# Performance work log

Measured on AMD Instinct MI355X. Metric: run time of the kernel, lower is better.

## Reference

```python
import jax, jax.numpy as jnp
import numpy as np

N = 200_000   # nodes
E = 6_400_000 # edges (avg degree 32)


def setup_inputs() -> dict:
    key = jax.random.key(0)
    k = jax.random.split(key, 6)
    x = jax.random.normal(k[0], (N, 2), dtype=jnp.float32)
    edge_index = jax.random.randint(k[1], (2, E), 0, N, dtype=jnp.int32)
    # GCNConv(2, 8) and GCNConv(8, 4) parameters (Glorot-ish init, zero bias as in PyG)
    W1 = jax.random.normal(k[2], (2, 8), dtype=jnp.float32) * (1.0 / np.sqrt(2.0))
    b1 = jnp.zeros((8,), dtype=jnp.float32)
    W2 = jax.random.normal(k[3], (8, 4), dtype=jnp.float32) * (1.0 / np.sqrt(8.0))
    b2 = jnp.zeros((4,), dtype=jnp.float32)
    return {"x": x, "edge_index": edge_index, "W1": W1, "b1": b1, "W2": W2, "b2": b2}


def _gcn_conv(x, src, dst, norm, W, b, n):
    # PyG GCNConv: linear transform, normalized gather/scatter-add, bias after aggregation
    h = x @ W                                   # [N, F_out]
    msg = h[src] * norm[:, None]                # gather + edge-wise scale, [E', F_out]
    agg = jax.ops.segment_sum(msg, dst, num_segments=n)  # scatter-add at targets
    return agg + b


def reference(x, edge_index, W1, b1, W2, b2):
    n = x.shape[0]
    # add self-loops (PyG default add_self_loops=True)
    loops = jnp.arange(n, dtype=edge_index.dtype)
    src = jnp.concatenate([edge_index[0], loops])
    dst = jnp.concatenate([edge_index[1], loops])
    # symmetric degree normalization: deg computed at targets with unit edge weights
    deg = jax.ops.segment_sum(jnp.ones_like(src, dtype=x.dtype), dst, num_segments=n)
    deg_inv_sqrt = jnp.where(deg > 0, jax.lax.rsqrt(jnp.maximum(deg, 1.0)), 0.0)
    norm = deg_inv_sqrt[src] * deg_inv_sqrt[dst]  # [E']

    h = jax.nn.relu(_gcn_conv(x, src, dst, norm, W1, b1, n))
    out = _gcn_conv(h, src, dst, norm, W2, b2, n)
    return out
```

## Files before the change

kernel.cpp:

```cpp
#include <hip/hip_runtime.h>


#define EPB   8192
#define PART  2048
#define LPBIT 11
#define SRCB  18
#define BC    4
#define RSTR  2049
#define STCAP 17408


__global__ __launch_bounds__(512) void countA_kernel(
    const int* __restrict__ dst, int* __restrict__ cntmat, int E, int P) {
    __shared__ int cnt[128];
    int tid = threadIdx.x;
    if (tid < 128) cnt[tid] = 0;
    __syncthreads();
    int nv4 = E >> 2;
    int b4 = (blockIdx.x * EPB) >> 2;
    int e4 = min(b4 + (EPB >> 2), nv4);
    const int4* d4 = (const int4*)dst;
    #pragma unroll
    for (int k = 0; k < (EPB >> 2); k += 512) {
        int i = b4 + k + tid;
        if (i < e4) {
            int4 d = d4[i];
            atomicAdd(&cnt[d.x >> LPBIT], 1);
            atomicAdd(&cnt[d.y >> LPBIT], 1);
            atomicAdd(&cnt[d.z >> LPBIT], 1);
            atomicAdd(&cnt[d.w >> LPBIT], 1);
        }
    }
    if (blockIdx.x == gridDim.x - 1) {
        int e = (nv4 << 2) + tid;
        if (e < E) atomicAdd(&cnt[dst[e] >> LPBIT], 1);
    }
    __syncthreads();
    int* row = cntmat + (size_t)blockIdx.x * P;
    if (tid < P) row[tid] = cnt[tid];
}

__global__ __launch_bounds__(256) void colscanA_kernel(
    int* __restrict__ cntmat, int* __restrict__ colTotal, int B, int P) {
    __shared__ int sdata[256];
    int p = blockIdx.x, tid = threadIdx.x;
    int v[4];
    int s = 0;
    #pragma unroll
    for (int k = 0; k < 4; k++) {
        int b = tid * 4 + k;
        v[k] = (b < B) ? cntmat[(size_t)b * P + p] : 0;
        s += v[k];
    }
    int x = s;
    sdata[tid] = x;
    __syncthreads();
    for (int off = 1; off < 256; off <<= 1) {
        int t = (tid >= off) ? sdata[tid - off] : 0;
        __syncthreads();
        x += t;
        sdata[tid] = x;
        __syncthreads();
    }
    int run = x - s;
    #pragma unroll
    for (int k = 0; k < 4; k++) {
        int b = tid * 4 + k;
        if (b < B) cntmat[(size_t)b * P + p] = run;
        run += v[k];
    }
    if (tid == 255) colTotal[p] = x;
}

__global__ __launch_bounds__(256) void totalscanA_kernel(
    const int* __restrict__ colTotal, int* __restrict__ colStart,
    int P, int E) {
    __shared__ int sdata[256];
    int tid = threadIdx.x;
    int v[4];
    int s = 0;
    #pragma unroll
    for (int k = 0; k < 4; k++) {
        int i = tid * 4 + k;
        v[k] = (i < P) ? colTotal[i] : 0;
        s += v[k];
    }
    int x = s;
    sdata[tid] = x;
    __syncthreads();
    for (int off = 1; off < 256; off <<= 1) {
        int t = (tid >= off) ? sdata[tid - off] : 0;
        __syncthreads();
        x += t;
        sdata[tid] = x;
        __syncthreads();
    }
    int run = x - s;
    #pragma unroll
    for (int k = 0; k < 4; k++) {
        int i = tid * 4 + k;
        if (i < P) colStart[i] = run;
        run += v[k];
    }
    if (tid == 0) colStart[P] = E;
}

__global__ __launch_bounds__(512) void scatterA_kernel(
    const int* __restrict__ src, const int* __restrict__ dst,
    const int* __restrict__ cntmat, const int* __restrict__ colStart,
    unsigned* __restrict__ packed, int E, int P) {
    __shared__ int cur[128];
    int tid = threadIdx.x;
    if (tid < P) cur[tid] = colStart[tid] + cntmat[(size_t)blockIdx.x * P + tid];
    __syncthreads();
    int nv4 = E >> 2;
    int b4 = (blockIdx.x * EPB) >> 2;
    int e4 = min(b4 + (EPB >> 2), nv4);
    const int4* d4 = (const int4*)dst;
    const int4* s4 = (const int4*)src;
    #pragma unroll
    for (int k = 0; k < (EPB >> 2); k += 512) {
        int i = b4 + k + tid;
        if (i < e4) {
            int4 d = d4[i];
            int4 sv = s4[i];
            int p0 = atomicAdd(&cur[d.x >> LPBIT], 1);
            packed[p0] = ((unsigned)(d.x & (PART - 1)) << SRCB) | (unsigned)sv.x;
            int p1 = atomicAdd(&cur[d.y >> LPBIT], 1);
            packed[p1] = ((unsigned)(d.y & (PART - 1)) << SRCB) | (unsigned)sv.y;
            int p2 = atomicAdd(&cur[d.z >> LPBIT], 1);
            packed[p2] = ((unsigned)(d.z & (PART - 1)) << SRCB) | (unsigned)sv.z;
            int p3 = atomicAdd(&cur[d.w >> LPBIT], 1);
            packed[p3] = ((unsigned)(d.w & (PART - 1)) << SRCB) | (unsigned)sv.w;
        }
    }
    if (blockIdx.x == gridDim.x - 1) {
        int e = (nv4 << 2) + tid;
        if (e < E) {
            int d = dst[e];
            int pos = atomicAdd(&cur[d >> LPBIT], 1);
            packed[pos] = ((unsigned)(d & (PART - 1)) << SRCB) | (unsigned)src[e];
        }
    }
}


__global__ __launch_bounds__(512) void localC_kernel(
    const unsigned* __restrict__ packed, const int* __restrict__ colStart,
    int* __restrict__ runStart, int* __restrict__ srcsorted) {
    __shared__ int hist[PART];
    __shared__ int sdata[512];
    __shared__ unsigned stage[STCAP];
    int tid = threadIdx.x;
    int dp = blockIdx.x >> 2, b = blockIdx.x & (BC - 1);
    int s0 = colStart[dp], len = colStart[dp + 1] - s0;
    int lo = s0 + (int)(((long long)len * b) / BC);
    int hi = s0 + (int)(((long long)len * (b + 1)) / BC);
    for (int k = tid; k < PART; k += 512) hist[k] = 0;
    __syncthreads();
    for (int i = lo + tid; i < hi; i += 512)
        atomicAdd(&hist[packed[i] >> SRCB], 1);
    __syncthreads();
    int off = tid * 4;
    int v0 = hist[off], v1 = hist[off + 1], v2 = hist[off + 2], v3 = hist[off + 3];
    int s = v0 + v1 + v2 + v3;
    int x = s;
    sdata[tid] = x;
    __syncthreads();
    for (int o = 1; o < 512; o <<= 1) {
        int t = (tid >= o) ? sdata[tid - o] : 0;
        __syncthreads();
        x += t;
        sdata[tid] = x;
        __syncthreads();
    }
    int run = x - s;
    int* rs = runStart + (size_t)(dp * BC + b) * RSTR;
    int c0 = lo + run, c1 = c0 + v0, c2 = c1 + v1, c3 = c2 + v2;
    rs[off] = c0; rs[off + 1] = c1; rs[off + 2] = c2; rs[off + 3] = c3;
    __syncthreads();
    hist[off] = c0; hist[off + 1] = c1; hist[off + 2] = c2; hist[off + 3] = c3;
    if (tid == 0) rs[PART] = hi;
    __syncthreads();
    int total = hi - lo;
    bool ovf = total > STCAP;
    for (int i = lo + tid; i < hi; i += 512) {
        unsigned w = packed[i];
        int pos = atomicAdd(&hist[w >> SRCB], 1);
        unsigned sv = w & ((1u << SRCB) - 1);
        if (!ovf) stage[pos - lo] = sv;
        else srcsorted[pos] = sv;
    }
    __syncthreads();
    if (!ovf)
        for (int j = tid; j < total; j += 512) srcsorted[lo + j] = (int)stage[j];
}


__global__ __launch_bounds__(512) void dinvg_kernel(
    const int* __restrict__ runStart, const float* __restrict__ x,
    float* __restrict__ dinv, float* __restrict__ g, int n) {
    int i = blockIdx.x * 512 + threadIdx.x;
    if (i >= n) return;
    int dp = i >> LPBIT, ld = i & (PART - 1);
    int deg = 0;
    #pragma unroll
    for (int b = 0; b < BC; b++) {
        const int* rs = runStart + (size_t)(dp * BC + b) * RSTR + ld;
        deg += rs[1] - rs[0];
    }
    float d = rsqrtf((float)deg + 1.0f);
    dinv[i] = d;
    float2 xv = ((const float2*)x)[i];
    ((float2*)g)[i] = make_float2(xv.x * d, xv.y * d);
}

__global__ __launch_bounds__(512) void agg1_kernel(
    const int* __restrict__ runStart, const int* __restrict__ srcsorted,
    const float* __restrict__ g, const float* __restrict__ dinv,
    const float* __restrict__ W1, const float* __restrict__ b1,
    const float* __restrict__ W2, float* __restrict__ hs2, int n) {
    int i = blockIdx.x * 512 + threadIdx.x;
    if (i >= n) return;
    int dp = i >> LPBIT, ld = i & (PART - 1);
    const float2* gp = (const float2*)g;
    float s0 = 0.0f, s1 = 0.0f;
    #pragma unroll
    for (int b = 0; b < BC; b++) {
        const int* rs = runStart + (size_t)(dp * BC + b) * RSTR + ld;
        int p0 = rs[0], p1 = rs[1];
        int p = p0;
        for (; p + 4 <= p1; p += 4) {
            int a = srcsorted[p], bb = srcsorted[p + 1];
            int c = srcsorted[p + 2], e = srcsorted[p + 3];
            float2 w0 = gp[a], w1 = gp[bb], w2 = gp[c], w3 = gp[e];
            s0 += w0.x + w1.x + w2.x + w3.x;
            s1 += w0.y + w1.y + w2.y + w3.y;
        }
        for (; p < p1; p++) {
            float2 w = gp[srcsorted[p]];
            s0 += w.x;
            s1 += w.y;
        }
    }
    float d = dinv[i];
    float2 gi = gp[i];
    s0 = (s0 + gi.x) * d;
    s1 = (s1 + gi.y) * d;
    float h[8];
    #pragma unroll
    for (int f = 0; f < 8; f++)
        h[f] = fmaxf(s0 * W1[f] + s1 * W1[8 + f] + b1[f], 0.0f);
    float oc[4];
    #pragma unroll
    for (int k = 0; k < 4; k++) {
        float a = 0.0f;
        #pragma unroll
        for (int f = 0; f < 8; f++) a += h[f] * W2[4 * f + k];
        oc[k] = a * d;
    }
    float4 o;
    o.x = oc[0]; o.y = oc[1]; o.z = oc[2]; o.w = oc[3];
    *(float4*)(hs2 + 4 * (size_t)i) = o;
}

__global__ __launch_bounds__(512) void agg2_kernel(
    const int* __restrict__ runStart, const int* __restrict__ srcsorted,
    const float* __restrict__ hs2, const float* __restrict__ dinv,
    const float* __restrict__ b2, float* __restrict__ out, int n) {
    int i = blockIdx.x * 512 + threadIdx.x;
    if (i >= n) return;
    int dp = i >> LPBIT, ld = i & (PART - 1);
    const float4* hp = (const float4*)hs2;
    float s0 = 0.0f, s1 = 0.0f, s2 = 0.0f, s3 = 0.0f;
    #pragma unroll
    for (int b = 0; b < BC; b++) {
        const int* rs = runStart + (size_t)(dp * BC + b) * RSTR + ld;
        int p0 = rs[0], p1 = rs[1];
        int p = p0;
        for (; p + 4 <= p1; p += 4) {
            int a = srcsorted[p], bb = srcsorted[p + 1];
            int c = srcsorted[p + 2], e = srcsorted[p + 3];
            float4 w0 = hp[a], w1 = hp[bb], w2 = hp[c], w3 = hp[e];
            s0 += w0.x + w1.x + w2.x + w3.x;
            s1 += w0.y + w1.y + w2.y + w3.y;
            s2 += w0.z + w1.z + w2.z + w3.z;
            s3 += w0.w + w1.w + w2.w + w3.w;
        }
        for (; p < p1; p++) {
            float4 w = hp[srcsorted[p]];
            s0 += w.x; s1 += w.y; s2 += w.z; s3 += w.w;
        }
    }
    float d = dinv[i];
    float4 hi2 = hp[i];
    float4 o;
    o.x = d * (s0 + hi2.x) + b2[0];
    o.y = d * (s1 + hi2.y) + b2[1];
    o.z = d * (s2 + hi2.z) + b2[2];
    o.w = d * (s3 + hi2.w) + b2[3];
    *(float4*)(out + 4 * (size_t)i) = o;
}

extern "C" void kernel_launch(void* const* d_in, const int* in_sizes, int n_in,
                              void* d_out, int out_size, void* d_ws, size_t ws_size,
                              hipStream_t stream) {
    const float* x   = (const float*)d_in[0];
    const int*   ei  = (const int*)d_in[1];
    const float* W1  = (const float*)d_in[2];
    const float* b1  = (const float*)d_in[3];
    const float* W2  = (const float*)d_in[4];
    const float* b2  = (const float*)d_in[5];
    float* out = (float*)d_out;

    const int n = in_sizes[0] / 2;
    const int E = in_sizes[1] / 2;
    const int* src = ei;
    const int* dst = ei + E;

    const int P  = (n + PART - 1) >> LPBIT;
    const int B1 = (E + EPB - 1) / EPB;

    int* ws = (int*)d_ws;
    int* colTotal = ws;
    int* colStart = ws + 1024;
    int* cntmatA  = ws + 2048;
    size_t cmsz = (((size_t)B1 * P) + 3) & ~(size_t)3;
    int* runStart = cntmatA + cmsz;
    size_t rssz = (((size_t)P * BC * RSTR) + 3) & ~(size_t)3;
    unsigned* packed = (unsigned*)(runStart + rssz);
    int* srcsorted = (int*)(packed + E);
    size_t nd = (size_t)P << LPBIT;
    float* dinv = (float*)packed;
    float* g    = dinv + nd;
    float* hs2  = g + 2 * nd;

    const int gN = (n + 511) / 512;

    countA_kernel    <<<B1, 512, 0, stream>>>(dst, cntmatA, E, P);
    colscanA_kernel  <<<P, 256, 0, stream>>>(cntmatA, colTotal, B1, P);
    totalscanA_kernel<<<1, 256, 0, stream>>>(colTotal, colStart, P, E);
    scatterA_kernel  <<<B1, 512, 0, stream>>>(src, dst, cntmatA, colStart, packed, E, P);
    localC_kernel    <<<P * BC, 512, 0, stream>>>(packed, colStart, runStart, srcsorted);
    dinvg_kernel     <<<gN, 512, 0, stream>>>(runStart, x, dinv, g, n);
    agg1_kernel      <<<gN, 512, 0, stream>>>(runStart, srcsorted, g, dinv, W1, b1, W2, hs2, n);
    agg2_kernel      <<<gN, 512, 0, stream>>>(runStart, srcsorted, hs2, dinv, b2, out, n);
}
```

Baseline: 247.6 us.

## Split each node's aggregation across four lanes, one per source bucket

The two aggregation kernels now assign four threads per destination node, each walking one of the BC=4 source-bucket runs. Partial sums are combined with xor shuffles, and each lane writes one output feature. The aim is four times more parallelism and more independent gathers in flight, which should hide latency better on the random-gather-bound loops. The cost is redundant per-node work (the dense W1/W2 math is repeated per lane), scalar instead of float4 stores, and more divergence when run lengths differ.

```diff
diff --git a/kernel.cpp b/kernel.cpp
--- a/kernel.cpp
+++ b/kernel.cpp
@@ -220,86 +220,79 @@
     const float* __restrict__ g, const float* __restrict__ dinv,
     const float* __restrict__ W1, const float* __restrict__ b1,
     const float* __restrict__ W2, float* __restrict__ hs2, int n) {
-    int i = blockIdx.x * 512 + threadIdx.x;
+    int t = blockIdx.x * 512 + threadIdx.x;
+    int i = t >> 2;
     if (i >= n) return;
+    int b = t & 3;
     int dp = i >> LPBIT, ld = i & (PART - 1);
+    const int* rs = runStart + (size_t)(dp * BC + b) * RSTR + ld;
+    int p0 = rs[0], p1 = rs[1];
     const float2* gp = (const float2*)g;
     float s0 = 0.0f, s1 = 0.0f;
-    #pragma unroll
-    for (int b = 0; b < BC; b++) {
-        const int* rs = runStart + (size_t)(dp * BC + b) * RSTR + ld;
-        int p0 = rs[0], p1 = rs[1];
-        int p = p0;
-        for (; p + 4 <= p1; p += 4) {
-            int a = srcsorted[p], bb = srcsorted[p + 1];
-            int c = srcsorted[p + 2], e = srcsorted[p + 3];
-            float2 w0 = gp[a], w1 = gp[bb], w2 = gp[c], w3 = gp[e];
-            s0 += w0.x + w1.x + w2.x + w3.x;
-            s1 += w0.y + w1.y + w2.y + w3.y;
-        }
-        for (; p < p1; p++) {
-            float2 w = gp[srcsorted[p]];
-            s0 += w.x;
-            s1 += w.y;
-        }
-    }
+    int p = p0;
+    for (; p + 4 <= p1; p += 4) {
+        int a = srcsorted[p], bb = srcsorted[p + 1];
+        int c = srcsorted[p + 2], e = srcsorted[p + 3];
+        float2 w0 = gp[a], w1 = gp[bb], w2 = gp[c], w3 = gp[e];
+        s0 += w0.x + w1.x + w2.x + w3.x;
+        s1 += w0.y + w1.y + w2.y + w3.y;
+    }
+    for (; p < p1; p++) {
+        float2 w = gp[srcsorted[p]];
+        s0 += w.x;
+        s1 += w.y;
+    }
+    s0 += __shfl_xor(s0, 1); s0 += __shfl_xor(s0, 2);
+    s1 += __shfl_xor(s1, 1); s1 += __shfl_xor(s1, 2);
     float d = dinv[i];
     float2 gi = gp[i];
     s0 = (s0 + gi.x) * d;
     s1 = (s1 + gi.y) * d;
-    float h[8];
-    #pragma unroll
-    for (int f = 0; f < 8; f++)
-        h[f] = fmaxf(s0 * W1[f] + s1 * W1[8 + f] + b1[f], 0.0f);
-    float oc[4];
-    #pragma unroll
-    for (int k = 0; k < 4; k++) {
-        float a = 0.0f;
-        #pragma unroll
-        for (int f = 0; f < 8; f++) a += h[f] * W2[4 * f + k];
-        oc[k] = a * d;
-    }
-    float4 o;
-    o.x = oc[0]; o.y = oc[1]; o.z = oc[2]; o.w = oc[3];
-    *(float4*)(hs2 + 4 * (size_t)i) = o;
+    float acc = 0.0f;
+    #pragma unroll
+    for (int f = 0; f < 8; f++) {
+        float h = fmaxf(s0 * W1[f] + s1 * W1[8 + f] + b1[f], 0.0f);
+        acc += h * W2[4 * f + b];
+    }
+    hs2[4 * (size_t)i + b] = acc * d;
 }
 
 __global__ __launch_bounds__(512) void agg2_kernel(
     const int* __restrict__ runStart, const int* __restrict__ srcsorted,
     const float* __restrict__ hs2, const float* __restrict__ dinv,
     const float* __restrict__ b2, float* __restrict__ out, int n) {
-    int i = blockIdx.x * 512 + threadIdx.x;
+    int t = blockIdx.x * 512 + threadIdx.x;
+    int i = t >> 2;
     if (i >= n) return;
+    int b = t & 3;
     int dp = i >> LPBIT, ld = i & (PART - 1);
+    const int* rs = runStart + (size_t)(dp * BC + b) * RSTR + ld;
+    int p0 = rs[0], p1 = rs[1];
     const float4* hp = (const float4*)hs2;
     float s0 = 0.0f, s1 = 0.0f, s2 = 0.0f, s3 = 0.0f;
-    #pragma unroll
-    for (int b = 0; b < BC; b++) {
-        const int* rs = runStart + (size_t)(dp * BC + b) * RSTR + ld;
-        int p0 = rs[0], p1 = rs[1];
-        int p = p0;
-        for (; p + 4 <= p1; p += 4) {
-            int a = srcsorted[p], bb = srcsorted[p + 1];
-            int c = srcsorted[p + 2], e = srcsorted[p + 3];
-            float4 w0 = hp[a], w1 = hp[bb], w2 = hp[c], w3 = hp[e];
-            s0 += w0.x + w1.x + w2.x + w3.x;
-            s1 += w0.y + w1.y + w2.y + w3.y;
-            s2 += w0.z + w1.z + w2.z + w3.z;
-            s3 += w0.w + w1.w + w2.w + w3.w;
-        }
-        for (; p < p1; p++) {
-            float4 w = hp[srcsorted[p]];
-            s0 += w.x; s1 += w.y; s2 += w.z; s3 += w.w;
-        }
-    }
+    int p = p0;
+    for (; p + 4 <= p1; p += 4) {
+        int a = srcsorted[p], bb = srcsorted[p + 1];
+        int c = srcsorted[p + 2], e = srcsorted[p + 3];
+        float4 w0 = hp[a], w1 = hp[bb], w2 = hp[c], w3 = hp[e];
+        s0 += w0.x + w1.x + w2.x + w3.x;
+        s1 += w0.y + w1.y + w2.y + w3.y;
+        s2 += w0.z + w1.z + w2.z + w3.z;
+        s3 += w0.w + w1.w + w2.w + w3.w;
+    }
+    for (; p < p1; p++) {
+        float4 w = hp[srcsorted[p]];
+        s0 += w.x; s1 += w.y; s2 += w.z; s3 += w.w;
+    }
+    s0 += __shfl_xor(s0, 1); s0 += __shfl_xor(s0, 2);
+    s1 += __shfl_xor(s1, 1); s1 += __shfl_xor(s1, 2);
+    s2 += __shfl_xor(s2, 1); s2 += __shfl_xor(s2, 2);
+    s3 += __shfl_xor(s3, 1); s3 += __shfl_xor(s3, 2);
     float d = dinv[i];
     float4 hi2 = hp[i];
-    float4 o;
-    o.x = d * (s0 + hi2.x) + b2[0];
-    o.y = d * (s1 + hi2.y) + b2[1];
-    o.z = d * (s2 + hi2.z) + b2[2];
-    o.w = d * (s3 + hi2.w) + b2[3];
-    *(float4*)(out + 4 * (size_t)i) = o;
+    float sb = (b == 0) ? s0 : (b == 1) ? s1 : (b == 2) ? s2 : s3;
+    float hb = (b == 0) ? hi2.x : (b == 1) ? hi2.y : (b == 2) ? hi2.z : hi2.w;
+    out[4 * (size_t)i + b] = d * (sb + hb) + b2[b];
 }
 
 extern "C" void kernel_launch(void* const* d_in, const int* in_sizes, int n_in,
@@ -335,7 +328,8 @@
     float* g    = dinv + nd;
     float* hs2  = g + 2 * nd;
 
-    const int gN = (n + 511) / 512;
+    const int gN  = (n + 511) / 512;
+    const int gN4 = (4 * n + 511) / 512;
 
     countA_kernel    <<<B1, 512, 0, stream>>>(dst, cntmatA, E, P);
     colscanA_kernel  <<<P, 256, 0, stream>>>(cntmatA, colTotal, B1, P);
@@ -343,6 +337,6 @@
     scatterA_kernel  <<<B1, 512, 0, stream>>>(src, dst, cntmatA, colStart, packed, E, P);
     localC_kernel    <<<P * BC, 512, 0, stream>>>(packed, colStart, runStart, srcsorted);
     dinvg_kernel     <<<gN, 512, 0, stream>>>(runStart, x, dinv, g, n);
-    agg1_kernel      <<<gN, 512, 0, stream>>>(runStart, srcsorted, g, dinv, W1, b1, W2, hs2, n);
-    agg2_kernel      <<<gN, 512, 0, stream>>>(runStart, srcsorted, hs2, dinv, b2, out, n);
-}
+    agg1_kernel      <<<gN4, 512, 0, stream>>>(runStart, srcsorted, g, dinv, W1, b1, W2, hs2, n);
+    agg2_kernel      <<<gN4, 512, 0, stream>>>(runStart, srcsorted, hs2, dinv, b2, out, n);
+}
```

Measured after the change: 248.5 us. No clear change (+0.4%).

## Switch aggregation from node-parallel CSR loops to edge-parallel segmented scans

Applied to the files above, without the earlier changes.

The sort output now keeps the packed destination-local id alongside the source id. Each aggregation is split into an edge-parallel kernel and a node kernel. The edge kernel finds each edge's partition by binary search over colStart, gathers the source features, reduces runs with equal destination using a wavefront shfl_up segmented scan, and emits one float atomicAdd per run. This removes the load imbalance and serial per-node loops of the node-parallel version, at the cost of extra accumulator zeroing, atomics, non-deterministic float summation order, and two more launches.

```diff
diff --git a/kernel.cpp b/kernel.cpp
--- a/kernel.cpp
+++ b/kernel.cpp
@@ -147,7 +147,7 @@
 
 __global__ __launch_bounds__(512) void localC_kernel(
     const unsigned* __restrict__ packed, const int* __restrict__ colStart,
-    int* __restrict__ runStart, int* __restrict__ srcsorted) {
+    int* __restrict__ runStart, int* __restrict__ sorted) {
     __shared__ int hist[PART];
     __shared__ int sdata[512];
     __shared__ unsigned stage[STCAP];
@@ -187,19 +187,19 @@
     for (int i = lo + tid; i < hi; i += 512) {
         unsigned w = packed[i];
         int pos = atomicAdd(&hist[w >> SRCB], 1);
-        unsigned sv = w & ((1u << SRCB) - 1);
-        if (!ovf) stage[pos - lo] = sv;
-        else srcsorted[pos] = sv;
+        if (!ovf) stage[pos - lo] = w;
+        else sorted[pos] = (int)w;
     }
     __syncthreads();
     if (!ovf)
-        for (int j = tid; j < total; j += 512) srcsorted[lo + j] = (int)stage[j];
+        for (int j = tid; j < total; j += 512) sorted[lo + j] = (int)stage[j];
 }
 
 
 __global__ __launch_bounds__(512) void dinvg_kernel(
     const int* __restrict__ runStart, const float* __restrict__ x,
-    float* __restrict__ dinv, float* __restrict__ g, int n) {
+    float* __restrict__ dinv, float* __restrict__ g,
+    float* __restrict__ acc1, float* __restrict__ acc2, int n) {
     int i = blockIdx.x * 512 + threadIdx.x;
     if (i >= n) return;
     int dp = i >> LPBIT, ld = i & (PART - 1);
@@ -213,93 +213,127 @@
     dinv[i] = d;
     float2 xv = ((const float2*)x)[i];
     ((float2*)g)[i] = make_float2(xv.x * d, xv.y * d);
-}
-
-__global__ __launch_bounds__(512) void agg1_kernel(
-    const int* __restrict__ runStart, const int* __restrict__ srcsorted,
-    const float* __restrict__ g, const float* __restrict__ dinv,
-    const float* __restrict__ W1, const float* __restrict__ b1,
-    const float* __restrict__ W2, float* __restrict__ hs2, int n) {
+    ((float2*)acc1)[i] = make_float2(0.0f, 0.0f);
+    ((float4*)acc2)[i] = make_float4(0.0f, 0.0f, 0.0f, 0.0f);
+}
+
+
+__global__ __launch_bounds__(512) void agg1e_kernel(
+    const int* __restrict__ sorted, const int* __restrict__ colStart,
+    const float* __restrict__ g, float* __restrict__ acc1, int E, int P) {
+    __shared__ int cs[132];
+    int tid = threadIdx.x;
+    for (int k = tid; k <= P; k += 512) cs[k] = colStart[k];
+    __syncthreads();
+    int e = blockIdx.x * 512 + tid;
+    int lane = tid & 63;
+    int sid = -1;
+    float s0 = 0.0f, s1 = 0.0f;
+    if (e < E) {
+        unsigned w = (unsigned)sorted[e];
+        int lo = 0, hi = P;
+        while (hi - lo > 1) { int mid = (lo + hi) >> 1; if (e >= cs[mid]) lo = mid; else hi = mid; }
+        sid = (lo << LPBIT) | (int)(w >> SRCB);
+        int src = (int)(w & ((1u << SRCB) - 1));
+        float2 gv = ((const float2*)g)[src];
+        s0 = gv.x; s1 = gv.y;
+    }
+    #pragma unroll
+    for (int off = 1; off < 64; off <<= 1) {
+        int ps = __shfl_up(sid, off);
+        float p0 = __shfl_up(s0, off);
+        float p1 = __shfl_up(s1, off);
+        if (lane >= off && ps == sid) { s0 += p0; s1 += p1; }
+    }
+    int ns = __shfl_down(sid, 1);
+    bool tail = (lane == 63) || (ns != sid);
+    if (tail && sid >= 0) {
+        atomicAdd(&acc1[2 * (size_t)sid],     s0);
+        atomicAdd(&acc1[2 * (size_t)sid + 1], s1);
+    }
+}
+
+__global__ __launch_bounds__(512) void agg2e_kernel(
+    const int* __restrict__ sorted, const int* __restrict__ colStart,
+    const float* __restrict__ hs2, float* __restrict__ acc2, int E, int P) {
+    __shared__ int cs[132];
+    int tid = threadIdx.x;
+    for (int k = tid; k <= P; k += 512) cs[k] = colStart[k];
+    __syncthreads();
+    int e = blockIdx.x * 512 + tid;
+    int lane = tid & 63;
+    int sid = -1;
+    float s0 = 0.0f, s1 = 0.0f, s2 = 0.0f, s3 = 0.0f;
+    if (e < E) {
+        unsigned w = (unsigned)sorted[e];
+        int lo = 0, hi = P;
+        while (hi - lo > 1) { int mid = (lo + hi) >> 1; if (e >= cs[mid]) lo = mid; else hi = mid; }
+        sid = (lo << LPBIT) | (int)(w >> SRCB);
+        int src = (int)(w & ((1u << SRCB) - 1));
+        float4 hv = ((const float4*)hs2)[src];
+        s0 = hv.x; s1 = hv.y; s2 = hv.z; s3 = hv.w;
+    }
+    #pragma unroll
+    for (int off = 1; off < 64; off <<= 1) {
+        int ps = __shfl_up(sid, off);
+        float p0 = __shfl_up(s0, off);
+        float p1 = __shfl_up(s1, off);
+        float p2 = __shfl_up(s2, off);
+        float p3 = __shfl_up(s3, off);
+        if (lane >= off && ps == sid) { s0 += p0; s1 += p1; s2 += p2; s3 += p3; }
+    }
+    int ns = __shfl_down(sid, 1);
+    bool tail = (lane == 63) || (ns != sid);
+    if (tail && sid >= 0) {
+        atomicAdd(&acc2[4 * (size_t)sid],     s0);
+        atomicAdd(&acc2[4 * (size_t)sid + 1], s1);
+        atomicAdd(&acc2[4 * (size_t)sid + 2], s2);
+        atomicAdd(&acc2[4 * (size_t)sid + 3], s3);
+    }
+}
+
+
+__global__ __launch_bounds__(512) void node1_kernel(
+    const float* __restrict__ acc1, const float* __restrict__ g,
+    const float* __restrict__ dinv, const float* __restrict__ W1,
+    const float* __restrict__ b1, const float* __restrict__ W2,
+    float* __restrict__ hs2, int n) {
     int i = blockIdx.x * 512 + threadIdx.x;
     if (i >= n) return;
-    int dp = i >> LPBIT, ld = i & (PART - 1);
-    const float2* gp = (const float2*)g;
-    float s0 = 0.0f, s1 = 0.0f;
-    #pragma unroll
-    for (int b = 0; b < BC; b++) {
-        const int* rs = runStart + (size_t)(dp * BC + b) * RSTR + ld;
-        int p0 = rs[0], p1 = rs[1];
-        int p = p0;
-        for (; p + 4 <= p1; p += 4) {
-            int a = srcsorted[p], bb = srcsorted[p + 1];
-            int c = srcsorted[p + 2], e = srcsorted[p + 3];
-            float2 w0 = gp[a], w1 = gp[bb], w2 = gp[c], w3 = gp[e];
-            s0 += w0.x + w1.x + w2.x + w3.x;
-            s1 += w0.y + w1.y + w2.y + w3.y;
-        }
-        for (; p < p1; p++) {
-            float2 w = gp[srcsorted[p]];
-            s0 += w.x;
-            s1 += w.y;
-        }
-    }
     float d = dinv[i];
-    float2 gi = gp[i];
-    s0 = (s0 + gi.x) * d;
-    s1 = (s1 + gi.y) * d;
-    float h[8];
-    #pragma unroll
-    for (int f = 0; f < 8; f++)
-        h[f] = fmaxf(s0 * W1[f] + s1 * W1[8 + f] + b1[f], 0.0f);
-    float oc[4];
-    #pragma unroll
-    for (int k = 0; k < 4; k++) {
-        float a = 0.0f;
-        #pragma unroll
-        for (int f = 0; f < 8; f++) a += h[f] * W2[4 * f + k];
-        oc[k] = a * d;
+    float2 a = ((const float2*)acc1)[i];
+    float2 gi = ((const float2*)g)[i];
+    float s0 = (a.x + gi.x) * d;
+    float s1 = (a.y + gi.y) * d;
+    float oc0 = 0.0f, oc1 = 0.0f, oc2 = 0.0f, oc3 = 0.0f;
+    #pragma unroll
+    for (int f = 0; f < 8; f++) {
+        float h = fmaxf(s0 * W1[f] + s1 * W1[8 + f] + b1[f], 0.0f);
+        oc0 += h * W2[4 * f];
+        oc1 += h * W2[4 * f + 1];
+        oc2 += h * W2[4 * f + 2];
+        oc3 += h * W2[4 * f + 3];
     }
     float4 o;
-    o.x = oc[0]; o.y = oc[1]; o.z = oc[2]; o.w = oc[3];
-    *(float4*)(hs2 + 4 * (size_t)i) = o;
-}
-
-__global__ __launch_bounds__(512) void agg2_kernel(
-    const int* __restrict__ runStart, const int* __restrict__ srcsorted,
-    const float* __restrict__ hs2, const float* __restrict__ dinv,
-    const float* __restrict__ b2, float* __restrict__ out, int n) {
+    o.x = oc0 * d; o.y = oc1 * d; o.z = oc2 * d; o.w = oc3 * d;
+    ((float4*)hs2)[i] = o;
+}
+
+__global__ __launch_bounds__(512) void node2_kernel(
+    const float* __restrict__ acc2, const float* __restrict__ hs2,
+    const float* __restrict__ dinv, const float* __restrict__ b2,
+    float* __restrict__ out, int n) {
     int i = blockIdx.x * 512 + threadIdx.x;
     if (i >= n) return;
-    int dp = i >> LPBIT, ld = i & (PART - 1);
-    const float4* hp = (const float4*)hs2;
-    float s0 = 0.0f, s1 = 0.0f, s2 = 0.0f, s3 = 0.0f;
-    #pragma unroll
-    for (int b = 0; b < BC; b++) {
-        const int* rs = runStart + (size_t)(dp * BC + b) * RSTR + ld;
-        int p0 = rs[0], p1 = rs[1];
-        int p = p0;
-        for (; p + 4 <= p1; p += 4) {
-            int a = srcsorted[p], bb = srcsorted[p + 1];
-            int c = srcsorted[p + 2], e = srcsorted[p + 3];
-            float4 w0 = hp[a], w1 = hp[bb], w2 = hp[c], w3 = hp[e];
-            s0 += w0.x + w1.x + w2.x + w3.x;
-            s1 += w0.y + w1.y + w2.y + w3.y;
-            s2 += w0.z + w1.z + w2.z + w3.z;
-            s3 += w0.w + w1.w + w2.w + w3.w;
-        }
-        for (; p < p1; p++) {
-            float4 w = hp[srcsorted[p]];
-            s0 += w.x; s1 += w.y; s2 += w.z; s3 += w.w;
-        }
-    }
     float d = dinv[i];
-    float4 hi2 = hp[i];
+    float4 a = ((const float4*)acc2)[i];
+    float4 hv = ((const float4*)hs2)[i];
     float4 o;
-    o.x = d * (s0 + hi2.x) + b2[0];
-    o.y = d * (s1 + hi2.y) + b2[1];
-    o.z = d * (s2 + hi2.z) + b2[2];
-    o.w = d * (s3 + hi2.w) + b2[3];
-    *(float4*)(out + 4 * (size_t)i) = o;
+    o.x = d * (a.x + hv.x) + b2[0];
+    o.y = d * (a.y + hv.y) + b2[1];
+    o.z = d * (a.z + hv.z) + b2[2];
+    o.w = d * (a.w + hv.w) + b2[3];
+    ((float4*)out)[i] = o;
 }
 
 extern "C" void kernel_launch(void* const* d_in, const int* in_sizes, int n_in,
@@ -329,20 +363,25 @@
     int* runStart = cntmatA + cmsz;
     size_t rssz = (((size_t)P * BC * RSTR) + 3) & ~(size_t)3;
     unsigned* packed = (unsigned*)(runStart + rssz);
-    int* srcsorted = (int*)(packed + E);
+    int* sorted = (int*)(packed + E);
     size_t nd = (size_t)P << LPBIT;
     float* dinv = (float*)packed;
     float* g    = dinv + nd;
     float* hs2  = g + 2 * nd;
+    float* acc1 = hs2 + 4 * nd;
+    float* acc2 = acc1 + 2 * nd;
 
     const int gN = (n + 511) / 512;
+    const int gE = (E + 511) / 512;
 
     countA_kernel    <<<B1, 512, 0, stream>>>(dst, cntmatA, E, P);
     colscanA_kernel  <<<P, 256, 0, stream>>>(cntmatA, colTotal, B1, P);
     totalscanA_kernel<<<1, 256, 0, stream>>>(colTotal, colStart, P, E);
     scatterA_kernel  <<<B1, 512, 0, stream>>>(src, dst, cntmatA, colStart, packed, E, P);
-    localC_kernel    <<<P * BC, 512, 0, stream>>>(packed, colStart, runStart, srcsorted);
-    dinvg_kernel     <<<gN, 512, 0, stream>>>(runStart, x, dinv, g, n);
-    agg1_kernel      <<<gN, 512, 0, stream>>>(runStart, srcsorted, g, dinv, W1, b1, W2, hs2, n);
-    agg2_kernel      <<<gN, 512, 0, stream>>>(runStart, srcsorted, hs2, dinv, b2, out, n);
-}
+    localC_kernel    <<<P * BC, 512, 0, stream>>>(packed, colStart, runStart, sorted);
+    dinvg_kernel     <<<gN, 512, 0, stream>>>(runStart, x, dinv, g, acc1, acc2, n);
+    agg1e_kernel     <<<gE, 512, 0, stream>>>(sorted, colStart, g, acc1, E, P);
+    node1_kernel     <<<gN, 512, 0, stream>>>(acc1, g, dinv, W1, b1, W2, hs2, n);
+    agg2e_kernel     <<<gE, 512, 0, stream>>>(sorted, colStart, hs2, acc2, E, P);
+    node2_kernel     <<<gN, 512, 0, stream>>>(acc2, hs2, dinv, b2, out, n);
+}
```

Measured after the change: 291.5 us. +17.7%, slower.

## Replace per-partition local sort with shared-memory atomic histogram aggregation

Applied to the files above, without the earlier changes.

Drops the second-level counting sort (localC) and the CSR-style runStart/srcsorted arrays. Degrees, layer-1 and layer-2 aggregations are now computed straight from the destination-bucketed packed edges. Each block accumulates into shared-memory float arrays indexed by local destination, writes per-sub-block partial sums, and separate combine kernels reduce the partials and apply the dense transforms. This removes a full sort pass and its writes, but it costs LDS float atomics per edge, reads packed three times, and adds partial-buffer traffic plus extra launches.

```diff
diff --git a/kernel.cpp b/kernel.cpp
--- a/kernel.cpp
+++ b/kernel.cpp
@@ -5,9 +5,9 @@
 #define PART  2048
 #define LPBIT 11
 #define SRCB  18
-#define BC    4
-#define RSTR  2049
-#define STCAP 17408
+#define SBD   6
+#define SB1   12
+#define SB2   6
 
 
 __global__ __launch_bounds__(512) void countA_kernel(
@@ -145,161 +145,152 @@
 }
 
 
-__global__ __launch_bounds__(512) void localC_kernel(
+__global__ __launch_bounds__(512) void deghist_kernel(
     const unsigned* __restrict__ packed, const int* __restrict__ colStart,
-    int* __restrict__ runStart, int* __restrict__ srcsorted) {
-    __shared__ int hist[PART];
-    __shared__ int sdata[512];
-    __shared__ unsigned stage[STCAP];
-    int tid = threadIdx.x;
-    int dp = blockIdx.x >> 2, b = blockIdx.x & (BC - 1);
-    int s0 = colStart[dp], len = colStart[dp + 1] - s0;
-    int lo = s0 + (int)(((long long)len * b) / BC);
-    int hi = s0 + (int)(((long long)len * (b + 1)) / BC);
-    for (int k = tid; k < PART; k += 512) hist[k] = 0;
-    __syncthreads();
-    for (int i = lo + tid; i < hi; i += 512)
-        atomicAdd(&hist[packed[i] >> SRCB], 1);
-    __syncthreads();
-    int off = tid * 4;
-    int v0 = hist[off], v1 = hist[off + 1], v2 = hist[off + 2], v3 = hist[off + 3];
-    int s = v0 + v1 + v2 + v3;
-    int x = s;
-    sdata[tid] = x;
-    __syncthreads();
-    for (int o = 1; o < 512; o <<= 1) {
-        int t = (tid >= o) ? sdata[tid - o] : 0;
-        __syncthreads();
-        x += t;
-        sdata[tid] = x;
-        __syncthreads();
-    }
-    int run = x - s;
-    int* rs = runStart + (size_t)(dp * BC + b) * RSTR;
-    int c0 = lo + run, c1 = c0 + v0, c2 = c1 + v1, c3 = c2 + v2;
-    rs[off] = c0; rs[off + 1] = c1; rs[off + 2] = c2; rs[off + 3] = c3;
-    __syncthreads();
-    hist[off] = c0; hist[off + 1] = c1; hist[off + 2] = c2; hist[off + 3] = c3;
-    if (tid == 0) rs[PART] = hi;
-    __syncthreads();
-    int total = hi - lo;
-    bool ovf = total > STCAP;
-    for (int i = lo + tid; i < hi; i += 512) {
-        unsigned w = packed[i];
-        int pos = atomicAdd(&hist[w >> SRCB], 1);
-        unsigned sv = w & ((1u << SRCB) - 1);
-        if (!ovf) stage[pos - lo] = sv;
-        else srcsorted[pos] = sv;
-    }
-    __syncthreads();
-    if (!ovf)
-        for (int j = tid; j < total; j += 512) srcsorted[lo + j] = (int)stage[j];
-}
-
+    int* __restrict__ degpart) {
+    __shared__ int cnt[PART];
+    int tid = threadIdx.x;
+    int p = blockIdx.x / SBD, sb = blockIdx.x - p * SBD;
+    int s0 = colStart[p], len = colStart[p + 1] - s0;
+    int lo = s0 + (int)(((long long)len * sb) / SBD);
+    int hi = s0 + (int)(((long long)len * (sb + 1)) / SBD);
+    for (int k = tid; k < PART; k += 512) cnt[k] = 0;
+    __syncthreads();
+    for (int e = lo + tid; e < hi; e += 512)
+        atomicAdd(&cnt[packed[e] >> SRCB], 1);
+    __syncthreads();
+    int* outp = degpart + (size_t)blockIdx.x * PART;
+    for (int k = tid; k < PART; k += 512) outp[k] = cnt[k];
+}
 
 __global__ __launch_bounds__(512) void dinvg_kernel(
-    const int* __restrict__ runStart, const float* __restrict__ x,
+    const int* __restrict__ degpart, const float* __restrict__ x,
     float* __restrict__ dinv, float* __restrict__ g, int n) {
     int i = blockIdx.x * 512 + threadIdx.x;
     if (i >= n) return;
-    int dp = i >> LPBIT, ld = i & (PART - 1);
+    int p = i >> LPBIT, ld = i & (PART - 1);
     int deg = 0;
     #pragma unroll
-    for (int b = 0; b < BC; b++) {
-        const int* rs = runStart + (size_t)(dp * BC + b) * RSTR + ld;
-        deg += rs[1] - rs[0];
-    }
+    for (int sb = 0; sb < SBD; sb++)
+        deg += degpart[(size_t)(p * SBD + sb) * PART + ld];
     float d = rsqrtf((float)deg + 1.0f);
     dinv[i] = d;
     float2 xv = ((const float2*)x)[i];
     ((float2*)g)[i] = make_float2(xv.x * d, xv.y * d);
 }
 
-__global__ __launch_bounds__(512) void agg1_kernel(
-    const int* __restrict__ runStart, const int* __restrict__ srcsorted,
-    const float* __restrict__ g, const float* __restrict__ dinv,
-    const float* __restrict__ W1, const float* __restrict__ b1,
-    const float* __restrict__ W2, float* __restrict__ hs2, int n) {
+
+__global__ __launch_bounds__(512) void agg1h_kernel(
+    const unsigned* __restrict__ packed, const int* __restrict__ colStart,
+    const float* __restrict__ g, float* __restrict__ part1) {
+    __shared__ float acc[2][PART];
+    int tid = threadIdx.x;
+    int p = blockIdx.x / SB1, sb = blockIdx.x - p * SB1;
+    int s0 = colStart[p], len = colStart[p + 1] - s0;
+    int lo = s0 + (int)(((long long)len * sb) / SB1);
+    int hi = s0 + (int)(((long long)len * (sb + 1)) / SB1);
+    for (int k = tid; k < 2 * PART; k += 512) ((float*)acc)[k] = 0.0f;
+    __syncthreads();
+    const float2* gp = (const float2*)g;
+    for (int e = lo + tid; e < hi; e += 512) {
+        unsigned w = packed[e];
+        int ld = (int)(w >> SRCB);
+        int src = (int)(w & ((1u << SRCB) - 1));
+        float2 gv = gp[src];
+        atomicAdd(&acc[0][ld], gv.x);
+        atomicAdd(&acc[1][ld], gv.y);
+    }
+    __syncthreads();
+    float* outp = part1 + (size_t)blockIdx.x * (2 * PART);
+    for (int k = tid; k < 2 * PART; k += 512) outp[k] = ((float*)acc)[k];
+}
+
+__global__ __launch_bounds__(512) void combine1_kernel(
+    const float* __restrict__ part1, const float* __restrict__ g,
+    const float* __restrict__ dinv, const float* __restrict__ W1,
+    const float* __restrict__ b1, const float* __restrict__ W2,
+    float* __restrict__ hs2, int n) {
     int i = blockIdx.x * 512 + threadIdx.x;
     if (i >= n) return;
-    int dp = i >> LPBIT, ld = i & (PART - 1);
-    const float2* gp = (const float2*)g;
+    int p = i >> LPBIT, ld = i & (PART - 1);
+    size_t base = (size_t)(p * SB1) * (2 * PART) + ld;
     float s0 = 0.0f, s1 = 0.0f;
     #pragma unroll
-    for (int b = 0; b < BC; b++) {
-        const int* rs = runStart + (size_t)(dp * BC + b) * RSTR + ld;
-        int p0 = rs[0], p1 = rs[1];
-        int p = p0;
-        for (; p + 4 <= p1; p += 4) {
-            int a = srcsorted[p], bb = srcsorted[p + 1];
-            int c = srcsorted[p + 2], e = srcsorted[p + 3];
-            float2 w0 = gp[a], w1 = gp[bb], w2 = gp[c], w3 = gp[e];
-            s0 += w0.x + w1.x + w2.x + w3.x;
-            s1 += w0.y + w1.y + w2.y + w3.y;
-        }
-        for (; p < p1; p++) {
-            float2 w = gp[srcsorted[p]];
-            s0 += w.x;
-            s1 += w.y;
-        }
+    for (int sb = 0; sb < SB1; sb++) {
+        s0 += part1[base + (size_t)sb * (2 * PART)];
+        s1 += part1[base + (size_t)sb * (2 * PART) + PART];
     }
     float d = dinv[i];
-    float2 gi = gp[i];
+    float2 gi = ((const float2*)g)[i];
     s0 = (s0 + gi.x) * d;
     s1 = (s1 + gi.y) * d;
-    float h[8];
-    #pragma unroll
-    for (int f = 0; f < 8; f++)
-        h[f] = fmaxf(s0 * W1[f] + s1 * W1[8 + f] + b1[f], 0.0f);
-    float oc[4];
-    #pragma unroll
-    for (int k = 0; k < 4; k++) {
-        float a = 0.0f;
-        #pragma unroll
-        for (int f = 0; f < 8; f++) a += h[f] * W2[4 * f + k];
-        oc[k] = a * d;
+    float oc0 = 0.0f, oc1 = 0.0f, oc2 = 0.0f, oc3 = 0.0f;
+    #pragma unroll
+    for (int f = 0; f < 8; f++) {
+        float h = fmaxf(s0 * W1[f] + s1 * W1[8 + f] + b1[f], 0.0f);
+        oc0 += h * W2[4 * f];
+        oc1 += h * W2[4 * f + 1];
+        oc2 += h * W2[4 * f + 2];
+        oc3 += h * W2[4 * f + 3];
     }
     float4 o;
-    o.x = oc[0]; o.y = oc[1]; o.z = oc[2]; o.w = oc[3];
-    *(float4*)(hs2 + 4 * (size_t)i) = o;
-}
-
-__global__ __launch_bounds__(512) void agg2_kernel(
-    const int* __restrict__ runStart, const int* __restrict__ srcsorted,
-    const float* __restrict__ hs2, const float* __restrict__ dinv,
-    const float* __restrict__ b2, float* __restrict__ out, int n) {
+    o.x = oc0 * d; o.y = oc1 * d; o.z = oc2 * d; o.w = oc3 * d;
+    ((float4*)hs2)[i] = o;
+}
+
+
+__global__ __launch_bounds__(512) void agg2h_kernel(
+    const unsigned* __restrict__ packed, const int* __restrict__ colStart,
+    const float* __restrict__ hs2, float* __restrict__ part2) {
+    __shared__ float acc[4][PART];
+    int tid = threadIdx.x;
+    int p = blockIdx.x / SB2, sb = blockIdx.x - p * SB2;
+    int s0 = colStart[p], len = colStart[p + 1] - s0;
+    int lo = s0 + (int)(((long long)len * sb) / SB2);
+    int hi = s0 + (int)(((long long)len * (sb + 1)) / SB2);
+    for (int k = tid; k < 4 * PART; k += 512) ((float*)acc)[k] = 0.0f;
+    __syncthreads();
+    const float4* hp = (const float4*)hs2;
+    for (int e = lo + tid; e < hi; e += 512) {
+        unsigned w = packed[e];
+        int ld = (int)(w >> SRCB);
+        int src = (int)(w & ((1u << SRCB) - 1));
+        float4 hv = hp[src];
+        atomicAdd(&acc[0][ld], hv.x);
+        atomicAdd(&acc[1][ld], hv.y);
+        atomicAdd(&acc[2][ld], hv.z);
+        atomicAdd(&acc[3][ld], hv.w);
+    }
+    __syncthreads();
+    float* outp = part2 + (size_t)blockIdx.x * (4 * PART);
+    for (int k = tid; k < 4 * PART; k += 512) outp[k] = ((float*)acc)[k];
+}
+
+__global__ __launch_bounds__(512) void combine2_kernel(
+    const float* __restrict__ part2, const float* __restrict__ hs2,
+    const float* __restrict__ dinv, const float* __restrict__ b2,
+    float* __restrict__ out, int n) {
     int i = blockIdx.x * 512 + threadIdx.x;
     if (i >= n) return;
-    int dp = i >> LPBIT, ld = i & (PART - 1);
-    const float4* hp = (const float4*)hs2;
+    int p = i >> LPBIT, ld = i & (PART - 1);
+    size_t base = (size_t)(p * SB2) * (4 * PART) + ld;
     float s0 = 0.0f, s1 = 0.0f, s2 = 0.0f, s3 = 0.0f;
     #pragma unroll
-    for (int b = 0; b < BC; b++) {
-        const int* rs = runStart + (size_t)(dp * BC + b) * RSTR + ld;
-        int p0 = rs[0], p1 = rs[1];
-        int p = p0;
-        for (; p + 4 <= p1; p += 4) {
-            int a = srcsorted[p], bb = srcsorted[p + 1];
-            int c = srcsorted[p + 2], e = srcsorted[p + 3];
-            float4 w0 = hp[a], w1 = hp[bb], w2 = hp[c], w3 = hp[e];
-            s0 += w0.x + w1.x + w2.x + w3.x;
-            s1 += w0.y + w1.y + w2.y + w3.y;
-            s2 += w0.z + w1.z + w2.z + w3.z;
-            s3 += w0.w + w1.w + w2.w + w3.w;
-        }
-        for (; p < p1; p++) {
-            float4 w = hp[srcsorted[p]];
-            s0 += w.x; s1 += w.y; s2 += w.z; s3 += w.w;
-        }
+    for (int sb = 0; sb < SB2; sb++) {
+        const float* q = part2 + base + (size_t)sb * (4 * PART);
+        s0 += q[0];
+        s1 += q[PART];
+        s2 += q[2 * PART];
+        s3 += q[3 * PART];
     }
     float d = dinv[i];
-    float4 hi2 = hp[i];
+    float4 hv = ((const float4*)hs2)[i];
     float4 o;
-    o.x = d * (s0 + hi2.x) + b2[0];
-    o.y = d * (s1 + hi2.y) + b2[1];
-    o.z = d * (s2 + hi2.z) + b2[2];
-    o.w = d * (s3 + hi2.w) + b2[3];
-    *(float4*)(out + 4 * (size_t)i) = o;
+    o.x = d * (s0 + hv.x) + b2[0];
+    o.y = d * (s1 + hv.y) + b2[1];
+    o.z = d * (s2 + hv.z) + b2[2];
+    o.w = d * (s3 + hv.w) + b2[3];
+    ((float4*)out)[i] = o;
 }
 
 extern "C" void kernel_launch(void* const* d_in, const int* in_sizes, int n_in,
@@ -326,14 +317,15 @@
     int* colStart = ws + 1024;
     int* cntmatA  = ws + 2048;
     size_t cmsz = (((size_t)B1 * P) + 3) & ~(size_t)3;
-    int* runStart = cntmatA + cmsz;
-    size_t rssz = (((size_t)P * BC * RSTR) + 3) & ~(size_t)3;
-    unsigned* packed = (unsigned*)(runStart + rssz);
-    int* srcsorted = (int*)(packed + E);
+    unsigned* packed = (unsigned*)(cntmatA + cmsz);
     size_t nd = (size_t)P << LPBIT;
-    float* dinv = (float*)packed;
+    float* dinv = (float*)(packed + E);
     float* g    = dinv + nd;
     float* hs2  = g + 2 * nd;
+    float* partial = hs2 + 4 * nd;
+    int*   degpart = (int*)partial;
+    float* part1   = partial;
+    float* part2   = partial;
 
     const int gN = (n + 511) / 512;
 
@@ -341,8 +333,10 @@
     colscanA_kernel  <<<P, 256, 0, stream>>>(cntmatA, colTotal, B1, P);
     totalscanA_kernel<<<1, 256, 0, stream>>>(colTotal, colStart, P, E);
     scatterA_kernel  <<<B1, 512, 0, stream>>>(src, dst, cntmatA, colStart, packed, E, P);
-    localC_kernel    <<<P * BC, 512, 0, stream>>>(packed, colStart, runStart, srcsorted);
-    dinvg_kernel     <<<gN, 512, 0, stream>>>(runStart, x, dinv, g, n);
-    agg1_kernel      <<<gN, 512, 0, stream>>>(runStart, srcsorted, g, dinv, W1, b1, W2, hs2, n);
-    agg2_kernel      <<<gN, 512, 0, stream>>>(runStart, srcsorted, hs2, dinv, b2, out, n);
-}
+    deghist_kernel   <<<P * SBD, 512, 0, stream>>>(packed, colStart, degpart);
+    dinvg_kernel     <<<gN, 512, 0, stream>>>(degpart, x, dinv, g, n);
+    agg1h_kernel     <<<P * SB1, 512, 0, stream>>>(packed, colStart, g, part1);
+    combine1_kernel  <<<gN, 512, 0, stream>>>(part1, g, dinv, W1, b1, W2, hs2, n);
+    agg2h_kernel     <<<P * SB2, 512, 0, stream>>>(packed, colStart, hs2, part2);
+    combine2_kernel  <<<gN, 512, 0, stream>>>(part2, hs2, dinv, b2, out, n);
+}
```

After: 399.5 us. 61.3% more time.
